# Kernel tuning notes

Measured on AMD Instinct MI355X. Metric: run time of the kernel, lower is better.

The kernel has to match this reference:

```python
import jax, jax.numpy as jnp
import numpy as np


def _gru_cell(x, h, W_ih, b_ih, W_hh, b_hh):
    # torch.nn.GRUCell math, gate order (r, z, n)
    gi = x @ W_ih.T + b_ih
    gh = h @ W_hh.T + b_hh
    ir, iz, inn = jnp.split(gi, 3, axis=-1)
    hr, hz, hn = jnp.split(gh, 3, axis=-1)
    r = jax.nn.sigmoid(ir + hr)
    zg = jax.nn.sigmoid(iz + hz)
    n = jnp.tanh(inn + r * hn)
    return (1.0 - zg) * n + zg * h


def setup_inputs() -> dict:
    key = jax.random.key(0)
    ks = jax.random.split(key, 16)
    B, T = 16384, 24
    MLP, Z, H = 1024, 32, 128
    NS, NP = 6, 2               # n_state, n_pred_state
    IN = MLP + Z + 2 * NP       # GRUCell input size = 1060
    f = lambda k, s, sc=1.0: jax.random.normal(k, s, dtype=jnp.float32) * sc
    return {
        "last_obs_state": f(ks[0], (B, NS)),
        "enc_h_feat": f(ks[1], (B, MLP)),
        "z": f(ks[2], (B, Z)),
        "sg": f(ks[3], (B, NP)),
        "fut_traj": f(ks[4], (T, B, NS)),
        # dec_hidden: Linear(mlp_dim+z_dim -> dec_h_dim)
        "W_dh": f(ks[5], (H, MLP + Z), 0.03),
        "b_dh": jnp.zeros((H,), jnp.float32),
        # to_vel: Linear(6 -> 2)
        "W_vel": f(ks[6], (NP, NS), 0.3),
        "b_vel": jnp.zeros((NP,), jnp.float32),
        # GRUCell weights
        "W_ih": f(ks[7], (3 * H, IN), 0.03),
        "b_ih": jnp.zeros((3 * H,), jnp.float32),
        "W_hh": f(ks[8], (3 * H, H), 0.08),
        "b_hh": jnp.zeros((3 * H,), jnp.float32),
        # fc_mu, fc_std: Linear(dec_h_dim -> 2)
        "W_mu": f(ks[9], (NP, H), 0.08),
        "b_mu": jnp.zeros((NP,), jnp.float32),
        "W_std": f(ks[10], (NP, H), 0.08),
        "b_std": jnp.zeros((NP,), jnp.float32),
    }


def reference(last_obs_state, enc_h_feat, z, sg, fut_traj,
              W_dh, b_dh, W_vel, b_vel, W_ih, b_ih, W_hh, b_hh,
              W_mu, b_mu, W_std, b_std):
    dt = 0.4 * 12
    zx = jnp.concatenate([enc_h_feat, z], axis=1)          # (B, mlp+z)
    h0 = zx @ W_dh.T + b_dh                                 # (B, H)
    a0 = last_obs_state @ W_vel.T + b_vel                   # (B, 2)
    rel = (sg - last_obs_state[:, :2]) / dt                 # (B, 2)
    # teacher forcing: a at step i is a0 for i=0, else fut_traj[i-1,:,2:4]
    a_seq = jnp.concatenate([a0[None], fut_traj[:-1, :, 2:4]], axis=0)  # (T,B,2)

    def step(h, a):
        x = jnp.concatenate([zx, a, rel], axis=1)           # (B, mlp+z+4)
        h = _gru_cell(x, h, W_ih, b_ih, W_hh, b_hh)
        mu = h @ W_mu.T + b_mu
        std = jnp.sqrt(jnp.exp(h @ W_std.T + b_std))
        return h, (mu, std)

    _, (mus, stds) = jax.lax.scan(step, h0, a_seq)
    return mus, stds  # each (T, B, 2): parameters of the returned Normal
```

## Files before the change

### kernel.cpp

```cpp
#include <hip/hip_runtime.h>

typedef __attribute__((ext_vector_type(4))) short short4v;
typedef __attribute__((ext_vector_type(8))) short short8;
typedef __attribute__((ext_vector_type(4))) float floatx4;

#define NB 16384
#define TT 24
#define HH 128
#define LDA 40
#define LDH 136

__device__ __forceinline__ float bf2f(unsigned short u) {
    union { unsigned int i; float f; } v; v.i = ((unsigned int)u) << 16; return v.f;
}
__device__ __forceinline__ unsigned short f2bf(float f) {
    union { float f; unsigned int i; } v; v.f = f;
    unsigned int x = v.i;
    unsigned int r = (x + 0x7fffu + ((x >> 16) & 1u)) >> 16;
    return (unsigned short)r;
}
__device__ __forceinline__ float fsig(float x) {
    return __fdividef(1.f, 1.f + __expf(-x));
}
__device__ __forceinline__ float ftanh(float x) {
    x = fminf(15.f, fmaxf(-15.f, x));
    float e = __expf(2.f * x);
    return __fdividef(e - 1.f, e + 1.f);
}

__device__ __forceinline__ float ldv(const void* base, size_t i, int isf32) {
    return isf32 ? ((const float*)base)[i] : bf2f(((const unsigned short*)base)[i]);
}
__device__ __forceinline__ short8 ld8(const void* base, size_t eoff, int isf32) {
    short8 r;
    if (isf32) {
        const float* p = (const float*)base + eoff;
        floatx4 a = *(const floatx4*)p;
        floatx4 b = *(const floatx4*)(p + 4);
        r[0] = (short)f2bf(a[0]); r[1] = (short)f2bf(a[1]);
        r[2] = (short)f2bf(a[2]); r[3] = (short)f2bf(a[3]);
        r[4] = (short)f2bf(b[0]); r[5] = (short)f2bf(b[1]);
        r[6] = (short)f2bf(b[2]); r[7] = (short)f2bf(b[3]);
    } else {
        r = *(const short8*)((const unsigned short*)base + eoff);
    }
    return r;
}
__device__ __forceinline__ short4v ld4(const void* base, size_t eoff, int isf32) {
    short4v r;
    if (isf32) {
        const float* p = (const float*)base + eoff;
        floatx4 a = *(const floatx4*)p;
        r[0] = (short)f2bf(a[0]); r[1] = (short)f2bf(a[1]);
        r[2] = (short)f2bf(a[2]); r[3] = (short)f2bf(a[3]);
    } else {
        r = *(const short4v*)((const unsigned short*)base + eoff);
    }
    return r;
}

__global__ __launch_bounds__(512, 2) void k_fused(
    const void* __restrict__ last, const void* __restrict__ enc,
    const void* __restrict__ zin, const void* __restrict__ sg,
    const void* __restrict__ fut, const void* __restrict__ W_dh,
    const void* __restrict__ b_dh, const void* __restrict__ W_vel,
    const void* __restrict__ b_vel, const void* __restrict__ W_ih,
    const void* __restrict__ b_ih, const void* __restrict__ W_hh,
    const void* __restrict__ b_hh, const void* __restrict__ W_mu,
    const void* __restrict__ b_mu, const void* __restrict__ W_std,
    const void* __restrict__ b_std, float* __restrict__ out) {
    __shared__ unsigned short As[64 * LDA];
    __shared__ unsigned short h_lds[64 * LDH];
    __shared__ float a_lds[64][2];
    __shared__ float rel_lds[64][2];
    __shared__ float wmu[2][HH], wstd[2][HH];
    __shared__ float bmuv[2], bstdv[2];

    const int tid = threadIdx.x;
    const int w = tid >> 6, lane = tid & 63;
    const int col = lane & 15, q = lane >> 4;
    const int b0 = blockIdx.x * 64;
    const int jc = w * 16 + col;

    int isf32;
    {
        const unsigned short* pu = (const unsigned short*)enc;
        unsigned short s = pu[(size_t)2 * (size_t)lane * 131072];
        int e = (s >> 7) & 0xFF;
        unsigned long long huge = __ballot(e >= 143);
        isf32 = (huge != 0ull) ? 1 : 0;
    }

    if (tid < 256) { int c = tid >> 7, k = tid & 127; wmu[c][k] = ldv(W_mu, c * HH + k, isf32); }
    else { int t2 = tid - 256; int c = t2 >> 7, k = t2 & 127; wstd[c][k] = ldv(W_std, c * HH + k, isf32); }
    if (tid < 2) { bmuv[tid] = ldv(b_mu, tid, isf32); bstdv[tid] = ldv(b_std, tid, isf32); }

    if (tid < 128) {
        int row = tid >> 1, c = tid & 1;
        int b = b0 + row;
        float s = ldv(b_vel, c, isf32);
#pragma unroll
        for (int s2 = 0; s2 < 6; s2++)
            s += ldv(last, b * 6 + s2, isf32) * ldv(W_vel, c * 6 + s2, isf32);
        a_lds[row][c] = s;
        rel_lds[row][c] = (ldv(sg, b * 2 + c, isf32) - ldv(last, b * 6 + c, isf32)) * (1.f / 4.8f);
    }

    floatx4 acc2[4][4];
#pragma unroll
    for (int i = 0; i < 4; i++)
#pragma unroll
        for (int j = 0; j < 4; j++) acc2[i][j] = (floatx4){0.f, 0.f, 0.f, 0.f};

    const int arow = tid >> 3, koff = (tid & 7) * 4;

    size_t woff[4];
#pragma unroll
    for (int g = 0; g < 3; g++) woff[g] = (size_t)(g * HH + jc) * 1060;
    const void* wbase[4] = {W_ih, W_ih, W_ih, W_dh};
    woff[3] = (size_t)jc * 1056;

    for (int ki = 0; ki < 33; ki++) {
        short4v av = (ki < 32)
            ? ld4(enc, (size_t)(b0 + arow) * 1024 + ki * 32 + koff, isf32)
            : ld4(zin, (size_t)(b0 + arow) * 32 + koff, isf32);
        __syncthreads();
        *(short4v*)(As + arow * LDA + koff) = av;
        __syncthreads();
        short8 af[4];
#pragma unroll
        for (int mt = 0; mt < 4; mt++)
            af[mt] = *(const short8*)(As + (mt * 16 + col) * LDA + q * 8);
#pragma unroll
        for (int gg = 0; gg < 4; gg++) {
            short8 bb = ld8(wbase[gg], woff[gg] + ki * 32 + q * 8, isf32);
#pragma unroll
            for (int mt = 0; mt < 4; mt++)
                acc2[mt][gg] = __builtin_amdgcn_mfma_f32_16x16x32_bf16(
                    af[mt], bb, acc2[mt][gg], 0, 0, 0);
        }
    }

    float bihg[3], wr0g[3], wr1g[3], wa0[3], wa1[3];
    float bhh_n;
#pragma unroll
    for (int g = 0; g < 3; g++) {
        const size_t rb = (size_t)(g * HH + jc) * 1060;
        bihg[g] = ldv(b_ih, g * HH + jc, isf32) + ((g < 2) ? ldv(b_hh, g * HH + jc, isf32) : 0.f);
        wr0g[g] = ldv(W_ih, rb + 1058, isf32);
        wr1g[g] = ldv(W_ih, rb + 1059, isf32);
        wa0[g] = ldv(W_ih, rb + 1056, isf32);
        wa1[g] = ldv(W_ih, rb + 1057, isf32);
    }
    bhh_n = ldv(b_hh, 2 * HH + jc, isf32);

    float greg[4][3][4];
    float hprev[4][4];
    const float bdh = ldv(b_dh, jc, isf32);
#pragma unroll
    for (int mt = 0; mt < 4; mt++) {
#pragma unroll
        for (int r = 0; r < 4; r++) {
            int blr = mt * 16 + q * 4 + r;
            float r0 = rel_lds[blr][0], r1 = rel_lds[blr][1];
#pragma unroll
            for (int g = 0; g < 3; g++)
                greg[mt][g][r] = acc2[mt][g][r] + bihg[g] + r0 * wr0g[g] + r1 * wr1g[g];
            float h0v = acc2[mt][3][r] + bdh;
            hprev[mt][r] = h0v;
            h_lds[blr * LDH + jc] = f2bf(h0v);
        }
    }

    short8 bfr[3][4];
#pragma unroll
    for (int g = 0; g < 3; g++)
#pragma unroll
        for (int kt = 0; kt < 4; kt++)
            bfr[g][kt] = ld8(W_hh, (size_t)(g * HH + jc) * HH + kt * 32 + q * 8, isf32);

    __syncthreads();

    for (int t = 0; t < TT; t++) {
        floatx4 acc[4][3];
#pragma unroll
        for (int mt = 0; mt < 4; mt++)
#pragma unroll
            for (int g = 0; g < 3; g++) acc[mt][g] = (floatx4){0.f, 0.f, 0.f, 0.f};
#pragma unroll
        for (int kt = 0; kt < 4; kt++) {
            short8 af2[4];
#pragma unroll
            for (int mt = 0; mt < 4; mt++)
                af2[mt] = *(const short8*)(h_lds + (mt * 16 + col) * LDH + kt * 32 + q * 8);
#pragma unroll
            for (int mt = 0; mt < 4; mt++)
#pragma unroll
                for (int g = 0; g < 3; g++)
                    acc[mt][g] = __builtin_amdgcn_mfma_f32_16x16x32_bf16(
                        af2[mt], bfr[g][kt], acc[mt][g], 0, 0, 0);
        }

#pragma unroll
        for (int mt = 0; mt < 4; mt++) {
#pragma unroll
            for (int r = 0; r < 4; r++) {
                int blr = mt * 16 + q * 4 + r;
                float a0v = a_lds[blr][0], a1v = a_lds[blr][1];
                float gir = greg[mt][0][r] + a0v * wa0[0] + a1v * wa1[0] + acc[mt][0][r];
                float giz = greg[mt][1][r] + a0v * wa0[1] + a1v * wa1[1] + acc[mt][1][r];
                float gin = greg[mt][2][r] + a0v * wa0[2] + a1v * wa1[2];
                float ghn = acc[mt][2][r] + bhh_n;
                float rg = fsig(gir);
                float zg = fsig(giz);
                float ng = ftanh(gin + rg * ghn);
                hprev[mt][r] = (1.f - zg) * ng + zg * hprev[mt][r];
            }
        }

        __syncthreads();

#pragma unroll
        for (int mt = 0; mt < 4; mt++)
#pragma unroll
            for (int r = 0; r < 4; r++)
                h_lds[(mt * 16 + q * 4 + r) * LDH + jc] = f2bf(hprev[mt][r]);
        if (tid < 128) {
            int row = tid >> 1, c = tid & 1;
            int b = b0 + row;
            a_lds[row][c] = ldv(fut, ((size_t)t * NB + b) * 6 + 2 + c, isf32);
        }

        __syncthreads();

        {
            int task = tid >> 1, part = tid & 1;
            int row = task >> 2, c = (task >> 1) & 1, kind = task & 1;
            const float* wv = kind ? wstd[c] : wmu[c];
            const unsigned short* hrow = h_lds + row * LDH + part * 64;
            float sum = 0.f;
#pragma unroll
            for (int k = 0; k < 64; k++) sum += bf2f(hrow[k]) * wv[part * 64 + k];
            sum += __shfl_xor(sum, 1);
            if (part == 0) {
                float val = sum + (kind ? bstdv[c] : bmuv[c]);
                if (kind) val = __expf(0.5f * val);
                out[(size_t)kind * (TT * NB * 2) + ((size_t)t * NB + (b0 + row)) * 2 + c] = val;
            }
        }
    }
}

extern "C" void kernel_launch(void* const* d_in, const int* in_sizes, int n_in,
                              void* d_out, int out_size, void* d_ws, size_t ws_size,
                              hipStream_t stream) {
    (void)d_ws; (void)ws_size; (void)in_sizes; (void)n_in; (void)out_size;
    float* out = (float*)d_out;

    k_fused<<<256, 512, 0, stream>>>(d_in[0], d_in[1], d_in[2], d_in[3], d_in[4],
                                     d_in[5], d_in[6], d_in[7], d_in[8], d_in[9],
                                     d_in[10], d_in[11], d_in[12], d_in[13], d_in[14],
                                     d_in[15], d_in[16], out);
}
```

Baseline: 366.0 us.

## Pre-convert weights to bf16, double-buffer LDS, and compute mu/std heads with MFMA

A new prep kernel converts W_ih/W_dh (packed to a 1056 stride), W_hh and the mu/std weights to bf16 in workspace. The main kernel no longer needs per-load fp32-to-bf16 conversion or the runtime dtype detection. The input projection loop double-buffers the A tile in LDS, cutting one barrier per k-step and prefetching the next slice. The recurrent loop double-buffers h and the teacher-forced action with an XOR-swizzled layout, dropping one barrier per timestep. The scalar mu/std dot products are replaced with MFMA, delayed by one step and overlapped with the next recurrence. In exchange it adds a second launch and assumes fp32 inputs.

```diff
diff --git a/kernel.cpp b/kernel.cpp
--- a/kernel.cpp
+++ b/kernel.cpp
@@ -9,6 +9,8 @@
 #define HH 128
 #define LDA 40
 #define LDH 136
+#define ASZ (64 * LDA)
+#define HSZ (64 * LDH)
 
 __device__ __forceinline__ float bf2f(unsigned short u) {
     union { unsigned int i; float f; } v; v.i = ((unsigned int)u) << 16; return v.f;
@@ -16,8 +18,7 @@
 __device__ __forceinline__ unsigned short f2bf(float f) {
     union { float f; unsigned int i; } v; v.f = f;
     unsigned int x = v.i;
-    unsigned int r = (x + 0x7fffu + ((x >> 16) & 1u)) >> 16;
-    return (unsigned short)r;
+    return (unsigned short)((x + 0x7fffu + ((x >> 16) & 1u)) >> 16);
 }
 __device__ __forceinline__ float fsig(float x) {
     return __fdividef(1.f, 1.f + __expf(-x));
@@ -27,54 +28,52 @@
     float e = __expf(2.f * x);
     return __fdividef(e - 1.f, e + 1.f);
 }
-
-__device__ __forceinline__ float ldv(const void* base, size_t i, int isf32) {
-    return isf32 ? ((const float*)base)[i] : bf2f(((const unsigned short*)base)[i]);
-}
-__device__ __forceinline__ short8 ld8(const void* base, size_t eoff, int isf32) {
-    short8 r;
-    if (isf32) {
-        const float* p = (const float*)base + eoff;
-        floatx4 a = *(const floatx4*)p;
-        floatx4 b = *(const floatx4*)(p + 4);
-        r[0] = (short)f2bf(a[0]); r[1] = (short)f2bf(a[1]);
-        r[2] = (short)f2bf(a[2]); r[3] = (short)f2bf(a[3]);
-        r[4] = (short)f2bf(b[0]); r[5] = (short)f2bf(b[1]);
-        r[6] = (short)f2bf(b[2]); r[7] = (short)f2bf(b[3]);
+__device__ __forceinline__ short4v pk4(floatx4 a) {
+    short4v r;
+    r[0] = (short)f2bf(a[0]); r[1] = (short)f2bf(a[1]);
+    r[2] = (short)f2bf(a[2]); r[3] = (short)f2bf(a[3]);
+    return r;
+}
+__device__ __forceinline__ int haddr(int row, int k) {
+    int chunk = (k >> 3) ^ ((row & 8) >> 2);
+    return row * LDH + (chunk << 3) + (k & 7);
+}
+
+__global__ void k_prep(const float* __restrict__ W_ih, const float* __restrict__ W_dh,
+                       const float* __restrict__ W_hh, const float* __restrict__ W_mu,
+                       const float* __restrict__ W_std, unsigned short* __restrict__ Wc,
+                       unsigned short* __restrict__ Whh, unsigned short* __restrict__ Wms) {
+    int blk = blockIdx.x;
+    if (blk < 512) {
+        const float* src = (blk < 384) ? (W_ih + (size_t)blk * 1060)
+                                       : (W_dh + (size_t)(blk - 384) * 1056);
+        unsigned short* dst = Wc + (size_t)blk * 1056;
+        for (int k = threadIdx.x; k < 1056; k += 256) dst[k] = f2bf(src[k]);
+    } else if (blk < 896) {
+        int r = blk - 512;
+        if (threadIdx.x < 128) Whh[r * 128 + threadIdx.x] = f2bf(W_hh[r * 128 + threadIdx.x]);
     } else {
-        r = *(const short8*)((const unsigned short*)base + eoff);
-    }
-    return r;
-}
-__device__ __forceinline__ short4v ld4(const void* base, size_t eoff, int isf32) {
-    short4v r;
-    if (isf32) {
-        const float* p = (const float*)base + eoff;
-        floatx4 a = *(const floatx4*)p;
-        r[0] = (short)f2bf(a[0]); r[1] = (short)f2bf(a[1]);
-        r[2] = (short)f2bf(a[2]); r[3] = (short)f2bf(a[3]);
-    } else {
-        r = *(const short4v*)((const unsigned short*)base + eoff);
-    }
-    return r;
+        for (int i = threadIdx.x; i < 512; i += 256) {
+            int r = i >> 7, k = i & 127;
+            Wms[i] = f2bf(r < 2 ? W_mu[r * 128 + k] : W_std[(r - 2) * 128 + k]);
+        }
+    }
 }
 
 __global__ __launch_bounds__(512, 2) void k_fused(
-    const void* __restrict__ last, const void* __restrict__ enc,
-    const void* __restrict__ zin, const void* __restrict__ sg,
-    const void* __restrict__ fut, const void* __restrict__ W_dh,
-    const void* __restrict__ b_dh, const void* __restrict__ W_vel,
-    const void* __restrict__ b_vel, const void* __restrict__ W_ih,
-    const void* __restrict__ b_ih, const void* __restrict__ W_hh,
-    const void* __restrict__ b_hh, const void* __restrict__ W_mu,
-    const void* __restrict__ b_mu, const void* __restrict__ W_std,
-    const void* __restrict__ b_std, float* __restrict__ out) {
-    __shared__ unsigned short As[64 * LDA];
-    __shared__ unsigned short h_lds[64 * LDH];
-    __shared__ float a_lds[64][2];
+    const float* __restrict__ last, const float* __restrict__ enc,
+    const float* __restrict__ zin, const float* __restrict__ sg,
+    const float* __restrict__ fut, const float* __restrict__ b_dh,
+    const float* __restrict__ W_vel, const float* __restrict__ b_vel,
+    const float* __restrict__ W_ih, const float* __restrict__ b_ih,
+    const float* __restrict__ b_hh, const float* __restrict__ b_mu,
+    const float* __restrict__ b_std, const unsigned short* __restrict__ Wc,
+    const unsigned short* __restrict__ Whh, const unsigned short* __restrict__ Wms,
+    float* __restrict__ out) {
+    __shared__ unsigned short As[2 * ASZ];
+    __shared__ unsigned short h2[2 * HSZ];
+    __shared__ float a_lds[2][64][2];
     __shared__ float rel_lds[64][2];
-    __shared__ float wmu[2][HH], wstd[2][HH];
-    __shared__ float bmuv[2], bstdv[2];
 
     const int tid = threadIdx.x;
     const int w = tid >> 6, lane = tid & 63;
@@ -82,28 +81,14 @@
     const int b0 = blockIdx.x * 64;
     const int jc = w * 16 + col;
 
-    int isf32;
-    {
-        const unsigned short* pu = (const unsigned short*)enc;
-        unsigned short s = pu[(size_t)2 * (size_t)lane * 131072];
-        int e = (s >> 7) & 0xFF;
-        unsigned long long huge = __ballot(e >= 143);
-        isf32 = (huge != 0ull) ? 1 : 0;
-    }
-
-    if (tid < 256) { int c = tid >> 7, k = tid & 127; wmu[c][k] = ldv(W_mu, c * HH + k, isf32); }
-    else { int t2 = tid - 256; int c = t2 >> 7, k = t2 & 127; wstd[c][k] = ldv(W_std, c * HH + k, isf32); }
-    if (tid < 2) { bmuv[tid] = ldv(b_mu, tid, isf32); bstdv[tid] = ldv(b_std, tid, isf32); }
-
     if (tid < 128) {
         int row = tid >> 1, c = tid & 1;
         int b = b0 + row;
-        float s = ldv(b_vel, c, isf32);
-#pragma unroll
-        for (int s2 = 0; s2 < 6; s2++)
-            s += ldv(last, b * 6 + s2, isf32) * ldv(W_vel, c * 6 + s2, isf32);
-        a_lds[row][c] = s;
-        rel_lds[row][c] = (ldv(sg, b * 2 + c, isf32) - ldv(last, b * 6 + c, isf32)) * (1.f / 4.8f);
+        float s = b_vel[c];
+#pragma unroll
+        for (int s2 = 0; s2 < 6; s2++) s += last[b * 6 + s2] * W_vel[c * 6 + s2];
+        a_lds[0][row][c] = s;
+        rel_lds[row][c] = (sg[b * 2 + c] - last[b * 6 + c]) * (1.f / 4.8f);
     }
 
     floatx4 acc2[4][4];
@@ -114,49 +99,53 @@
 
     const int arow = tid >> 3, koff = (tid & 7) * 4;
 
-    size_t woff[4];
-#pragma unroll
-    for (int g = 0; g < 3; g++) woff[g] = (size_t)(g * HH + jc) * 1060;
-    const void* wbase[4] = {W_ih, W_ih, W_ih, W_dh};
-    woff[3] = (size_t)jc * 1056;
+    {
+        floatx4 a0 = *(const floatx4*)(enc + (size_t)(b0 + arow) * 1024 + koff);
+        *(short4v*)(As + arow * LDA + koff) = pk4(a0);
+    }
+    __syncthreads();
 
     for (int ki = 0; ki < 33; ki++) {
-        short4v av = (ki < 32)
-            ? ld4(enc, (size_t)(b0 + arow) * 1024 + ki * 32 + koff, isf32)
-            : ld4(zin, (size_t)(b0 + arow) * 32 + koff, isf32);
-        __syncthreads();
-        *(short4v*)(As + arow * LDA + koff) = av;
-        __syncthreads();
+        const int cur = ki & 1, nxt = cur ^ 1;
+        floatx4 an;
+        if (ki < 32) {
+            an = (ki + 1 < 32)
+                ? *(const floatx4*)(enc + (size_t)(b0 + arow) * 1024 + (ki + 1) * 32 + koff)
+                : *(const floatx4*)(zin + (size_t)(b0 + arow) * 32 + koff);
+        }
+        short8 bb[4];
+#pragma unroll
+        for (int gg = 0; gg < 4; gg++)
+            bb[gg] = *(const short8*)(Wc + (size_t)(gg * 128 + jc) * 1056 + ki * 32 + q * 8);
         short8 af[4];
 #pragma unroll
         for (int mt = 0; mt < 4; mt++)
-            af[mt] = *(const short8*)(As + (mt * 16 + col) * LDA + q * 8);
-#pragma unroll
-        for (int gg = 0; gg < 4; gg++) {
-            short8 bb = ld8(wbase[gg], woff[gg] + ki * 32 + q * 8, isf32);
+            af[mt] = *(const short8*)(As + cur * ASZ + (mt * 16 + col) * LDA + q * 8);
+#pragma unroll
+        for (int gg = 0; gg < 4; gg++)
 #pragma unroll
             for (int mt = 0; mt < 4; mt++)
                 acc2[mt][gg] = __builtin_amdgcn_mfma_f32_16x16x32_bf16(
-                    af[mt], bb, acc2[mt][gg], 0, 0, 0);
-        }
-    }
-
-    float bihg[3], wr0g[3], wr1g[3], wa0[3], wa1[3];
-    float bhh_n;
+                    af[mt], bb[gg], acc2[mt][gg], 0, 0, 0);
+        if (ki < 32) *(short4v*)(As + nxt * ASZ + arow * LDA + koff) = pk4(an);
+        __syncthreads();
+    }
+
+    float bihg[3], wr0g[3], wr1g[3], wa0[3], wa1[3], bhh_n;
 #pragma unroll
     for (int g = 0; g < 3; g++) {
         const size_t rb = (size_t)(g * HH + jc) * 1060;
-        bihg[g] = ldv(b_ih, g * HH + jc, isf32) + ((g < 2) ? ldv(b_hh, g * HH + jc, isf32) : 0.f);
-        wr0g[g] = ldv(W_ih, rb + 1058, isf32);
-        wr1g[g] = ldv(W_ih, rb + 1059, isf32);
-        wa0[g] = ldv(W_ih, rb + 1056, isf32);
-        wa1[g] = ldv(W_ih, rb + 1057, isf32);
-    }
-    bhh_n = ldv(b_hh, 2 * HH + jc, isf32);
+        bihg[g] = b_ih[g * HH + jc] + ((g < 2) ? b_hh[g * HH + jc] : 0.f);
+        wa0[g] = W_ih[rb + 1056];
+        wa1[g] = W_ih[rb + 1057];
+        wr0g[g] = W_ih[rb + 1058];
+        wr1g[g] = W_ih[rb + 1059];
+    }
+    bhh_n = b_hh[2 * HH + jc];
 
     float greg[4][3][4];
     float hprev[4][4];
-    const float bdh = ldv(b_dh, jc, isf32);
+    const float bdh = b_dh[jc];
 #pragma unroll
     for (int mt = 0; mt < 4; mt++) {
 #pragma unroll
@@ -168,7 +157,7 @@
                 greg[mt][g][r] = acc2[mt][g][r] + bihg[g] + r0 * wr0g[g] + r1 * wr1g[g];
             float h0v = acc2[mt][3][r] + bdh;
             hprev[mt][r] = h0v;
-            h_lds[blr * LDH + jc] = f2bf(h0v);
+            h2[haddr(blr, jc)] = f2bf(h0v);
         }
     }
 
@@ -177,28 +166,64 @@
     for (int g = 0; g < 3; g++)
 #pragma unroll
         for (int kt = 0; kt < 4; kt++)
-            bfr[g][kt] = ld8(W_hh, (size_t)(g * HH + jc) * HH + kt * 32 + q * 8, isf32);
+            bfr[g][kt] = *(const short8*)(Whh + (size_t)(g * HH + jc) * HH + kt * 32 + q * 8);
+
+    short8 msf[4];
+    float msbias = 0.f;
+    if (w < 2) {
+#pragma unroll
+        for (int kt = 0; kt < 4; kt++)
+            msf[kt] = (col < 4) ? *(const short8*)(Wms + col * 128 + kt * 32 + q * 8)
+                                : (short8){0, 0, 0, 0, 0, 0, 0, 0};
+        if (col < 4) msbias = (col >= 2) ? b_std[col & 1] : b_mu[col & 1];
+    }
 
     __syncthreads();
 
     for (int t = 0; t < TT; t++) {
+        const unsigned short* hc = h2 + (t & 1) * HSZ;
+        unsigned short* hn = h2 + ((t + 1) & 1) * HSZ;
+
         floatx4 acc[4][3];
+        floatx4 accms[2];
 #pragma unroll
         for (int mt = 0; mt < 4; mt++)
 #pragma unroll
             for (int g = 0; g < 3; g++) acc[mt][g] = (floatx4){0.f, 0.f, 0.f, 0.f};
+        accms[0] = (floatx4){0.f, 0.f, 0.f, 0.f};
+        accms[1] = (floatx4){0.f, 0.f, 0.f, 0.f};
+
 #pragma unroll
         for (int kt = 0; kt < 4; kt++) {
             short8 af2[4];
 #pragma unroll
             for (int mt = 0; mt < 4; mt++)
-                af2[mt] = *(const short8*)(h_lds + (mt * 16 + col) * LDH + kt * 32 + q * 8);
+                af2[mt] = *(const short8*)(hc + haddr(mt * 16 + col, kt * 32 + q * 8));
 #pragma unroll
             for (int mt = 0; mt < 4; mt++)
 #pragma unroll
                 for (int g = 0; g < 3; g++)
                     acc[mt][g] = __builtin_amdgcn_mfma_f32_16x16x32_bf16(
                         af2[mt], bfr[g][kt], acc[mt][g], 0, 0, 0);
+            if (w < 2 && t > 0) {
+#pragma unroll
+                for (int mtl = 0; mtl < 2; mtl++)
+                    accms[mtl] = __builtin_amdgcn_mfma_f32_16x16x32_bf16(
+                        af2[w * 2 + mtl], msf[kt], accms[mtl], 0, 0, 0);
+            }
+        }
+
+        if (w < 2 && t > 0 && col < 4) {
+            int kind = col >> 1, c = col & 1;
+#pragma unroll
+            for (int mtl = 0; mtl < 2; mtl++)
+#pragma unroll
+                for (int r = 0; r < 4; r++) {
+                    float val = accms[mtl][r] + msbias;
+                    if (kind) val = __expf(0.5f * val);
+                    int b = b0 + (w * 2 + mtl) * 16 + q * 4 + r;
+                    out[(size_t)kind * (TT * NB * 2) + (size_t)(t - 1) * NB * 2 + b * 2 + c] = val;
+                }
         }
 
 #pragma unroll
@@ -206,7 +231,7 @@
 #pragma unroll
             for (int r = 0; r < 4; r++) {
                 int blr = mt * 16 + q * 4 + r;
-                float a0v = a_lds[blr][0], a1v = a_lds[blr][1];
+                float a0v = a_lds[t & 1][blr][0], a1v = a_lds[t & 1][blr][1];
                 float gir = greg[mt][0][r] + a0v * wa0[0] + a1v * wa1[0] + acc[mt][0][r];
                 float giz = greg[mt][1][r] + a0v * wa0[1] + a1v * wa1[1] + acc[mt][1][r];
                 float gin = greg[mt][2][r] + a0v * wa0[2] + a1v * wa1[2];
@@ -218,35 +243,44 @@
             }
         }
 
-        __syncthreads();
-
 #pragma unroll
         for (int mt = 0; mt < 4; mt++)
 #pragma unroll
             for (int r = 0; r < 4; r++)
-                h_lds[(mt * 16 + q * 4 + r) * LDH + jc] = f2bf(hprev[mt][r]);
+                hn[haddr(mt * 16 + q * 4 + r, jc)] = f2bf(hprev[mt][r]);
         if (tid < 128) {
             int row = tid >> 1, c = tid & 1;
-            int b = b0 + row;
-            a_lds[row][c] = ldv(fut, ((size_t)t * NB + b) * 6 + 2 + c, isf32);
+            a_lds[(t + 1) & 1][row][c] = fut[((size_t)t * NB + b0 + row) * 6 + 2 + c];
         }
 
         __syncthreads();
-
-        {
-            int task = tid >> 1, part = tid & 1;
-            int row = task >> 2, c = (task >> 1) & 1, kind = task & 1;
-            const float* wv = kind ? wstd[c] : wmu[c];
-            const unsigned short* hrow = h_lds + row * LDH + part * 64;
-            float sum = 0.f;
-#pragma unroll
-            for (int k = 0; k < 64; k++) sum += bf2f(hrow[k]) * wv[part * 64 + k];
-            sum += __shfl_xor(sum, 1);
-            if (part == 0) {
-                float val = sum + (kind ? bstdv[c] : bmuv[c]);
-                if (kind) val = __expf(0.5f * val);
-                out[(size_t)kind * (TT * NB * 2) + ((size_t)t * NB + (b0 + row)) * 2 + c] = val;
+    }
+
+    if (w < 2) {
+        const unsigned short* hc = h2 + (TT & 1) * HSZ;
+        floatx4 accms[2];
+        accms[0] = (floatx4){0.f, 0.f, 0.f, 0.f};
+        accms[1] = (floatx4){0.f, 0.f, 0.f, 0.f};
+#pragma unroll
+        for (int kt = 0; kt < 4; kt++) {
+#pragma unroll
+            for (int mtl = 0; mtl < 2; mtl++) {
+                short8 af2 = *(const short8*)(hc + haddr((w * 2 + mtl) * 16 + col, kt * 32 + q * 8));
+                accms[mtl] = __builtin_amdgcn_mfma_f32_16x16x32_bf16(
+                    af2, msf[kt], accms[mtl], 0, 0, 0);
             }
+        }
+        if (col < 4) {
+            int kind = col >> 1, c = col & 1;
+#pragma unroll
+            for (int mtl = 0; mtl < 2; mtl++)
+#pragma unroll
+                for (int r = 0; r < 4; r++) {
+                    float val = accms[mtl][r] + msbias;
+                    if (kind) val = __expf(0.5f * val);
+                    int b = b0 + (w * 2 + mtl) * 16 + q * 4 + r;
+                    out[(size_t)kind * (TT * NB * 2) + (size_t)(TT - 1) * NB * 2 + b * 2 + c] = val;
+                }
         }
     }
 }
@@ -254,11 +288,32 @@
 extern "C" void kernel_launch(void* const* d_in, const int* in_sizes, int n_in,
                               void* d_out, int out_size, void* d_ws, size_t ws_size,
                               hipStream_t stream) {
-    (void)d_ws; (void)ws_size; (void)in_sizes; (void)n_in; (void)out_size;
+    (void)in_sizes; (void)n_in; (void)out_size; (void)ws_size;
+    const float* last  = (const float*)d_in[0];
+    const float* enc   = (const float*)d_in[1];
+    const float* zin   = (const float*)d_in[2];
+    const float* sg    = (const float*)d_in[3];
+    const float* fut   = (const float*)d_in[4];
+    const float* W_dh  = (const float*)d_in[5];
+    const float* b_dh  = (const float*)d_in[6];
+    const float* W_vel = (const float*)d_in[7];
+    const float* b_vel = (const float*)d_in[8];
+    const float* W_ih  = (const float*)d_in[9];
+    const float* b_ih  = (const float*)d_in[10];
+    const float* W_hh  = (const float*)d_in[11];
+    const float* b_hh  = (const float*)d_in[12];
+    const float* W_mu  = (const float*)d_in[13];
+    const float* b_mu  = (const float*)d_in[14];
+    const float* W_std = (const float*)d_in[15];
+    const float* b_std = (const float*)d_in[16];
     float* out = (float*)d_out;
 
-    k_fused<<<256, 512, 0, stream>>>(d_in[0], d_in[1], d_in[2], d_in[3], d_in[4],
-                                     d_in[5], d_in[6], d_in[7], d_in[8], d_in[9],
-                                     d_in[10], d_in[11], d_in[12], d_in[13], d_in[14],
-                                     d_in[15], d_in[16], out);
-}
+    char* ws = (char*)d_ws;
+    unsigned short* Wc  = (unsigned short*)ws;
+    unsigned short* Whh = (unsigned short*)(ws + 1081344);
+    unsigned short* Wms = (unsigned short*)(ws + 1179648);
+
+    k_prep<<<897, 256, 0, stream>>>(W_ih, W_dh, W_hh, W_mu, W_std, Wc, Whh, Wms);
+    k_fused<<<256, 512, 0, stream>>>(last, enc, zin, sg, fut, b_dh, W_vel, b_vel,
+                                     W_ih, b_ih, b_hh, b_mu, b_std, Wc, Whh, Wms, out);
+}
```

New measurement: 570.7 us. 55.9% more time.
